# Performance work log

Hardware: AMD Instinct MI355X
Metric: run time of the kernel (lower is better)

The kernel has to match this reference:

```python
import jax, jax.numpy as jnp
import numpy as np

N = 100000
E = 1600000
H = 8
C = 16
DIM = 128
EDGE_DIM = 32


def setup_inputs() -> dict:
    key = jax.random.key(0)
    ks = jax.random.split(key, 7)
    s = 1.0 / np.sqrt(DIM)
    return {
        "x": jax.random.normal(ks[0], (N, DIM), dtype=jnp.float32),
        "edge_index": jax.random.randint(ks[1], (2, E), 0, N, dtype=jnp.int32),
        "edge_attr": jax.random.normal(ks[2], (E, EDGE_DIM), dtype=jnp.float32),
        "Wq": jax.random.normal(ks[3], (H * C, DIM), dtype=jnp.float32) * s,
        "Wk": jax.random.normal(ks[4], (H * C, DIM), dtype=jnp.float32) * s,
        "Wv": jax.random.normal(ks[5], (H * C, DIM), dtype=jnp.float32) * s,
        "We": jax.random.normal(ks[6], (H, EDGE_DIM), dtype=jnp.float32) * (1.0 / np.sqrt(EDGE_DIM)),
    }


def reference(x, edge_index, edge_attr, Wq, Wk, Wv, We):
    # Node projections: [N, H, C]
    q = (x @ Wq.T).reshape(N, H, C)
    k = (x @ Wk.T).reshape(N, H, C)
    v = (x @ Wv.T).reshape(N, H, C)

    src, dst = edge_index[0], edge_index[1]

    # Per-edge attention logits with edge bias: [E, H]
    edge_bias = edge_attr @ We.T
    scores = jnp.einsum("ehc,ehc->eh", q[dst], k[src]) / np.sqrt(C) + edge_bias

    # Numerically-stable segment softmax over destination groups
    seg_max = jax.ops.segment_max(scores, dst, num_segments=N)  # [N, H]
    ex = jnp.exp(scores - seg_max[dst])
    denom = jax.ops.segment_sum(ex, dst, num_segments=N)  # [N, H]
    alpha = ex / denom[dst]  # [E, H]

    # Scale gathered values and scatter-add to destinations
    msgs = v[src] * alpha[:, :, None]  # [E, H, C]
    out = jax.ops.segment_sum(msgs, dst, num_segments=N)  # [N, H, C]
    return out.reshape(N, H * C)
```

## Files before the change

### kernel.cpp

```cpp
#include <hip/hip_runtime.h>


typedef unsigned int uint32;
typedef unsigned short ushort16;

__device__ inline unsigned short f2bf(float f) {
    uint32 u = __float_as_uint(f);
    uint32 r = u + 0x7fffu + ((u >> 16) & 1u);
    return (unsigned short)(r >> 16);
}

__global__ __launch_bounds__(256) void qkv_count_kernel(
    const float* __restrict__ x,
    const float* __restrict__ Wq,
    const float* __restrict__ Wk,
    const float* __restrict__ Wv,
    const int* __restrict__ edge_index,
    float* __restrict__ q,
    unsigned short* __restrict__ kbf,
    unsigned short* __restrict__ vbf,
    int* __restrict__ counts,
    int N, int E)
{
    if (blockIdx.y == 6) {
        int idx = blockIdx.x * 256 + threadIdx.x;
        if (idx * 4 + 3 < E) {
            int4 d4 = ((const int4*)(edge_index + E))[idx];
            atomicAdd(&counts[d4.x], 1);
            atomicAdd(&counts[d4.y], 1);
            atomicAdd(&counts[d4.z], 1);
            atomicAdd(&counts[d4.w], 1);
        } else {
            for (int e = idx * 4; e < E; ++e)
                atomicAdd(&counts[edge_index[(size_t)E + e]], 1);
        }
        return;
    }

    const int nb = blockIdx.x * 64;
    const int cb = blockIdx.y * 64;
    const float* __restrict__ W = (cb < 128) ? Wq : (cb < 256) ? Wk : Wv;
    const int wrow0 = cb & 127;

    __shared__ float As[16][68];
    __shared__ float Bs[16][68];

    const int tid = threadIdx.x;
    const int tx = tid & 15;
    const int ty = tid >> 4;

    float acc[4][4] = {};

    const int lrow = tid >> 2;
    const int lk   = (tid & 3) * 4;
    const int n_load = nb + lrow;

    for (int k0 = 0; k0 < 128; k0 += 16) {
        float4 a = make_float4(0.f, 0.f, 0.f, 0.f);
        if (n_load < N)
            a = *(const float4*)(x + (size_t)n_load * 128 + k0 + lk);
        float4 b = *(const float4*)(W + (size_t)(wrow0 + lrow) * 128 + k0 + lk);
        As[lk + 0][lrow] = a.x; As[lk + 1][lrow] = a.y;
        As[lk + 2][lrow] = a.z; As[lk + 3][lrow] = a.w;
        Bs[lk + 0][lrow] = b.x; Bs[lk + 1][lrow] = b.y;
        Bs[lk + 2][lrow] = b.z; Bs[lk + 3][lrow] = b.w;
        __syncthreads();
#pragma unroll
        for (int kk = 0; kk < 16; ++kk) {
            float4 av = *(const float4*)&As[kk][ty * 4];
            float4 bv = *(const float4*)&Bs[kk][tx * 4];
            float avr[4] = {av.x, av.y, av.z, av.w};
            float bvr[4] = {bv.x, bv.y, bv.z, bv.w};
#pragma unroll
            for (int i = 0; i < 4; ++i)
#pragma unroll
                for (int j = 0; j < 4; ++j)
                    acc[i][j] = fmaf(avr[i], bvr[j], acc[i][j]);
        }
        __syncthreads();
    }

#pragma unroll
    for (int i = 0; i < 4; ++i) {
        int n = nb + ty * 4 + i;
        if (n >= N) continue;
        if (cb < 128) {
            float4 o = make_float4(acc[i][0], acc[i][1], acc[i][2], acc[i][3]);
            *(float4*)(q + (size_t)n * 128 + wrow0 + tx * 4) = o;
        } else {
            unsigned short* kv = (cb < 256) ? kbf : vbf;
            ushort4 o;
            o.x = f2bf(acc[i][0]); o.y = f2bf(acc[i][1]);
            o.z = f2bf(acc[i][2]); o.w = f2bf(acc[i][3]);
            *(ushort4*)(kv + (size_t)n * 128 + wrow0 + tx * 4) = o;
        }
    }
}

__global__ __launch_bounds__(256) void scan_pass1(
    const int* __restrict__ counts, int* __restrict__ blocksums, int N)
{
    __shared__ int red[256];
    int base = blockIdx.x * 512;
    int t = threadIdx.x;
    int s = 0;
    if (base + t < N)       s += counts[base + t];
    if (base + 256 + t < N) s += counts[base + 256 + t];
    red[t] = s;
    __syncthreads();
    for (int off = 128; off > 0; off >>= 1) {
        if (t < off) red[t] += red[t + off];
        __syncthreads();
    }
    if (t == 0) blocksums[blockIdx.x] = red[0];
}

__global__ __launch_bounds__(256) void scan_pass2(
    const int* __restrict__ blocksums, int* __restrict__ blockbase, int NB)
{
    __shared__ int sc[256];
    int t = threadIdx.x;
    int v = (t < NB) ? blocksums[t] : 0;
    sc[t] = v;
    __syncthreads();
    for (int off = 1; off < 256; off <<= 1) {
        int tmp = (t >= off) ? sc[t - off] : 0;
        __syncthreads();
        sc[t] += tmp;
        __syncthreads();
    }
    if (t < NB) blockbase[t] = sc[t] - v;
}

__global__ __launch_bounds__(256) void scan_pass3(
    const int* __restrict__ counts, const int* __restrict__ blockbase,
    int* __restrict__ offsets, int* __restrict__ cursor, int N)
{
    __shared__ int sc[256];
    int base = blockIdx.x * 512;
    int t = threadIdx.x;
    int i0 = base + 2 * t, i1 = i0 + 1;
    int c0 = (i0 < N) ? counts[i0] : 0;
    int c1 = (i1 < N) ? counts[i1] : 0;
    int pair = c0 + c1;
    sc[t] = pair;
    __syncthreads();
    for (int off = 1; off < 256; off <<= 1) {
        int tmp = (t >= off) ? sc[t - off] : 0;
        __syncthreads();
        sc[t] += tmp;
        __syncthreads();
    }
    int ex = sc[t] - pair + blockbase[blockIdx.x];
    if (i0 < N) { offsets[i0] = ex;      cursor[i0] = ex; }
    if (i1 < N) { offsets[i1] = ex + c0; cursor[i1] = ex + c0; }
}

__global__ __launch_bounds__(256) void scatter_kernel(
    const int* __restrict__ edge_index,
    int* __restrict__ cursor,
    int2* __restrict__ perm,
    int E)
{
    int e = blockIdx.x * 256 + threadIdx.x;
    if (e >= E) return;
    int s = edge_index[e];
    int d = edge_index[(size_t)E + e];
    int pos = atomicAdd(&cursor[d], 1);
    perm[pos] = make_int2(s, e);
}

__global__ __launch_bounds__(256) void attn_fused_kernel(
    const float* __restrict__ q,
    const unsigned short* __restrict__ kbf,
    const unsigned short* __restrict__ vbf,
    const float* __restrict__ edge_attr,
    const float* __restrict__ We,
    const int* __restrict__ offsets,
    const int* __restrict__ counts,
    const int2* __restrict__ perm,
    float* __restrict__ out,
    int N)
{
    const int d    = blockIdx.x * 4 + (threadIdx.x >> 6);
    const int lane = threadIdx.x & 63;
    if (d >= N) return;
    const int h = lane >> 3;
    const int j = lane & 7;

    const float4 we4 = *(const float4*)(We + h * 32 + j * 4);
    const float2 q2  = *(const float2*)(q + (size_t)d * 128 + lane * 2);

    const int start = offsets[d];
    const int cnt   = counts[d];

    float denom = 0.f, accx = 0.f, accy = 0.f;

    for (int i0 = 0; i0 < cnt; i0 += 64) {
        int m = min(64, cnt - i0);
        int2 pv = make_int2(0, 0);
        if (lane < m) pv = perm[start + i0 + lane];

        int src = __shfl(pv.x, 0), e = __shfl(pv.y, 0);
        uint32 kk2 = *(const uint32*)(kbf + (size_t)src * 128 + lane * 2);
        uint32 vv2 = *(const uint32*)(vbf + (size_t)src * 128 + lane * 2);
        float4 ea  = *(const float4*)(edge_attr + (size_t)e * 32 + j * 4);

        for (int t = 0; t < m; ++t) {
            uint32 ck = kk2, cv = vv2;
            float4 cea = ea;
            if (t + 1 < m) {
                int ns = __shfl(pv.x, t + 1), ne = __shfl(pv.y, t + 1);
                kk2 = *(const uint32*)(kbf + (size_t)ns * 128 + lane * 2);
                vv2 = *(const uint32*)(vbf + (size_t)ns * 128 + lane * 2);
                ea  = *(const float4*)(edge_attr + (size_t)ne * 32 + j * 4);
            }
            float kx = __uint_as_float(ck << 16);
            float ky = __uint_as_float(ck & 0xffff0000u);
            float part = 0.25f * (q2.x * kx + q2.y * ky)
                       + cea.x * we4.x + cea.y * we4.y
                       + cea.z * we4.z + cea.w * we4.w;
            part += __shfl_xor(part, 1);
            part += __shfl_xor(part, 2);
            part += __shfl_xor(part, 4);
            float ev = __expf(part);
            denom += ev;
            float vx = __uint_as_float(cv << 16);
            float vy = __uint_as_float(cv & 0xffff0000u);
            accx = fmaf(ev, vx, accx);
            accy = fmaf(ev, vy, accy);
        }
    }

    float inv = denom > 0.f ? 1.f / denom : 0.f;
    *(float2*)(out + (size_t)d * 128 + lane * 2) = make_float2(accx * inv, accy * inv);
}

extern "C" void kernel_launch(void* const* d_in, const int* in_sizes, int n_in,
                              void* d_out, int out_size, void* d_ws, size_t ws_size,
                              hipStream_t stream) {
    const float* x          = (const float*)d_in[0];
    const int*   edge_index = (const int*)d_in[1];
    const float* edge_attr  = (const float*)d_in[2];
    const float* Wq         = (const float*)d_in[3];
    const float* Wk         = (const float*)d_in[4];
    const float* Wv         = (const float*)d_in[5];
    const float* We         = (const float*)d_in[6];
    float* out = (float*)d_out;

    const int N = in_sizes[0] / 128;
    const int E = in_sizes[1] / 2;

    float* q = (float*)d_ws;
    unsigned short* kbf = (unsigned short*)(q + (size_t)N * 128);
    unsigned short* vbf = kbf + (size_t)N * 128;
    int2* perm = (int2*)(vbf + (size_t)N * 128);
    int* counts    = (int*)(perm + E);
    int* offsets   = counts + N;
    int* cursor    = offsets + N;
    int* blocksums = cursor + N;
    int* blockbase = blocksums + 256;

    hipMemsetAsync(counts, 0, (size_t)N * sizeof(int), stream);

    const int nxb = (N + 63) / 64;
    dim3 g1(nxb, 7);
    qkv_count_kernel<<<g1, 256, 0, stream>>>(x, Wq, Wk, Wv, edge_index,
                                             q, kbf, vbf, counts, N, E);

    const int NB = (N + 511) / 512;
    scan_pass1<<<NB, 256, 0, stream>>>(counts, blocksums, N);
    scan_pass2<<<1, 256, 0, stream>>>(blocksums, blockbase, NB);
    scan_pass3<<<NB, 256, 0, stream>>>(counts, blockbase, offsets, cursor, N);

    scatter_kernel<<<(E + 255) / 256, 256, 0, stream>>>(edge_index, cursor,
                                                        perm, E);

    attn_fused_kernel<<<(N + 3) / 4, 256, 0, stream>>>(
        q, kbf, vbf, edge_attr, We, offsets, counts, perm, out, N);
}
```

Measured before the change: 770.2 us.

## Deepen gather prefetch to two 4-edge groups in attention aggregation loop

The per-destination aggregation loop now keeps two groups of four edges' K/V/edge_attr loads in flight and software-pipelines them, where before it prefetched only one edge ahead. Edge indices are read with readlane instead of shfl, and the 0.25 scale is folded into q. The aim is to hide gather latency by raising memory-level parallelism. The cost is extra registers, which can lower occupancy.

```diff
diff --git a/kernel.cpp b/kernel.cpp
--- a/kernel.cpp
+++ b/kernel.cpp
@@ -2,7 +2,6 @@
 
 
 typedef unsigned int uint32;
-typedef unsigned short ushort16;
 
 __device__ inline unsigned short f2bf(float f) {
     uint32 u = __float_as_uint(f);
@@ -190,46 +189,70 @@
 
     const float4 we4 = *(const float4*)(We + h * 32 + j * 4);
     const float2 q2  = *(const float2*)(q + (size_t)d * 128 + lane * 2);
+    const float qx = q2.x * 0.25f;
+    const float qy = q2.y * 0.25f;
 
     const int start = offsets[d];
     const int cnt   = counts[d];
 
     float denom = 0.f, accx = 0.f, accy = 0.f;
 
+    const int laneb = lane * 4;
+    const char* kbp = (const char*)kbf;
+    const char* vbp = (const char*)vbf;
+
     for (int i0 = 0; i0 < cnt; i0 += 64) {
-        int m = min(64, cnt - i0);
+        const int m = min(64, cnt - i0);
         int2 pv = make_int2(0, 0);
         if (lane < m) pv = perm[start + i0 + lane];
 
-        int src = __shfl(pv.x, 0), e = __shfl(pv.y, 0);
-        uint32 kk2 = *(const uint32*)(kbf + (size_t)src * 128 + lane * 2);
-        uint32 vv2 = *(const uint32*)(vbf + (size_t)src * 128 + lane * 2);
-        float4 ea  = *(const float4*)(edge_attr + (size_t)e * 32 + j * 4);
-
-        for (int t = 0; t < m; ++t) {
-            uint32 ck = kk2, cv = vv2;
-            float4 cea = ea;
-            if (t + 1 < m) {
-                int ns = __shfl(pv.x, t + 1), ne = __shfl(pv.y, t + 1);
-                kk2 = *(const uint32*)(kbf + (size_t)ns * 128 + lane * 2);
-                vv2 = *(const uint32*)(vbf + (size_t)ns * 128 + lane * 2);
-                ea  = *(const float4*)(edge_attr + (size_t)ne * 32 + j * 4);
-            }
-            float kx = __uint_as_float(ck << 16);
-            float ky = __uint_as_float(ck & 0xffff0000u);
-            float part = 0.25f * (q2.x * kx + q2.y * ky)
-                       + cea.x * we4.x + cea.y * we4.y
-                       + cea.z * we4.z + cea.w * we4.w;
-            part += __shfl_xor(part, 1);
-            part += __shfl_xor(part, 2);
-            part += __shfl_xor(part, 4);
-            float ev = __expf(part);
-            denom += ev;
-            float vx = __uint_as_float(cv << 16);
-            float vy = __uint_as_float(cv & 0xffff0000u);
-            accx = fmaf(ev, vx, accx);
-            accy = fmaf(ev, vy, accy);
-        }
+        uint32 ka[4], va[4]; float4 ea[4];
+        uint32 kc[4], vc[4]; float4 ec[4];
+
+#define LOADG(AK, AV, AE, T0)                                                  \
+        _Pragma("unroll")                                                      \
+        for (int u = 0; u < 4; ++u) {                                          \
+            int t = (T0) + u;                                                  \
+            if (t < m) {                                                       \
+                int src = __builtin_amdgcn_readlane(pv.x, t);                  \
+                int e   = __builtin_amdgcn_readlane(pv.y, t);                  \
+                AK[u] = *(const uint32*)(kbp + ((size_t)src << 8) + laneb);    \
+                AV[u] = *(const uint32*)(vbp + ((size_t)src << 8) + laneb);    \
+                AE[u] = *(const float4*)(edge_attr + (size_t)e * 32 + j * 4);  \
+            }                                                                  \
+        }
+
+#define COMPG(AK, AV, AE, T0)                                                  \
+        _Pragma("unroll")                                                      \
+        for (int u = 0; u < 4; ++u) {                                          \
+            int t = (T0) + u;                                                  \
+            if (t < m) {                                                       \
+                float kx = __uint_as_float(AK[u] << 16);                       \
+                float ky = __uint_as_float(AK[u] & 0xffff0000u);               \
+                float4 ce = AE[u];                                             \
+                float part = qx * kx + qy * ky                                 \
+                           + ce.x * we4.x + ce.y * we4.y                       \
+                           + ce.z * we4.z + ce.w * we4.w;                      \
+                part += __shfl_xor(part, 1);                                   \
+                part += __shfl_xor(part, 2);                                   \
+                part += __shfl_xor(part, 4);                                   \
+                float ev = __expf(part);                                       \
+                denom += ev;                                                   \
+                accx = fmaf(ev, __uint_as_float(AV[u] << 16), accx);           \
+                accy = fmaf(ev, __uint_as_float(AV[u] & 0xffff0000u), accy);   \
+            }                                                                  \
+        }
+
+        LOADG(ka, va, ea, 0)
+        LOADG(kc, vc, ec, 4)
+        for (int t0 = 0; t0 < m; t0 += 8) {
+            COMPG(ka, va, ea, t0)
+            LOADG(ka, va, ea, t0 + 8)
+            COMPG(kc, vc, ec, t0 + 4)
+            LOADG(kc, vc, ec, t0 + 12)
+        }
+#undef LOADG
+#undef COMPG
     }
 
     float inv = denom > 0.f ? 1.f / denom : 0.f;
```

Measured after the change: 835.9 us. +8.5%, slower.

## Precompute per-edge bias in projection kernel and use DPP for head reductions

Applied to the files above, without the earlier changes.

Adds a grid slice to the projection kernel that computes the edge_attr·We bias for every edge with coalesced streaming reads and stores it as an E×8 array. The attention kernel then gathers one float per edge-head instead of a float4 of edge_attr per lane and drops the per-edge dot product. Cross-lane shuffles in the head reduction are replaced by DPP moves. This needs extra workspace and an additional large write and read of the bias array, and falls back to the old path if the workspace is too small.

```diff
diff --git a/kernel.cpp b/kernel.cpp
--- a/kernel.cpp
+++ b/kernel.cpp
@@ -2,12 +2,17 @@
 
 
 typedef unsigned int uint32;
-typedef unsigned short ushort16;
 
 __device__ inline unsigned short f2bf(float f) {
     uint32 u = __float_as_uint(f);
     uint32 r = u + 0x7fffu + ((u >> 16) & 1u);
     return (unsigned short)(r >> 16);
+}
+
+template <int CTRL>
+__device__ inline float dpp_mov(float v) {
+    return __int_as_float(__builtin_amdgcn_update_dpp(
+        0, __float_as_int(v), CTRL, 0xF, 0xF, true));
 }
 
 __global__ __launch_bounds__(256) void qkv_count_kernel(
@@ -15,10 +20,13 @@
     const float* __restrict__ Wq,
     const float* __restrict__ Wk,
     const float* __restrict__ Wv,
+    const float* __restrict__ We,
+    const float* __restrict__ edge_attr,
     const int* __restrict__ edge_index,
     float* __restrict__ q,
     unsigned short* __restrict__ kbf,
     unsigned short* __restrict__ vbf,
+    float* __restrict__ ebias,
     int* __restrict__ counts,
     int N, int E)
 {
@@ -33,6 +41,32 @@
         } else {
             for (int e = idx * 4; e < E; ++e)
                 atomicAdd(&counts[edge_index[(size_t)E + e]], 1);
+        }
+        return;
+    }
+
+    if (blockIdx.y == 7) {
+        const int t  = threadIdx.x;
+        const int h  = t & 7;
+        const int er = t >> 3;
+        float4 wreg[8];
+#pragma unroll
+        for (int i = 0; i < 8; ++i)
+            wreg[i] = *(const float4*)(We + h * 32 + i * 4);
+        const int e0 = blockIdx.x * 1024;
+        for (int it = 0; it < 32; ++it) {
+            int e = e0 + it * 32 + er;
+            if (e < E) {
+                const float* ea = edge_attr + (size_t)e * 32;
+                float s = 0.f;
+#pragma unroll
+                for (int i = 0; i < 8; ++i) {
+                    float4 a = *(const float4*)(ea + i * 4);
+                    float4 w = wreg[i];
+                    s += a.x * w.x + a.y * w.y + a.z * w.z + a.w * w.w;
+                }
+                ebias[(size_t)e * 8 + h] = s;
+            }
         }
         return;
     }
@@ -170,10 +204,12 @@
     perm[pos] = make_int2(s, e);
 }
 
+template <bool USE_BIAS>
 __global__ __launch_bounds__(256) void attn_fused_kernel(
     const float* __restrict__ q,
     const unsigned short* __restrict__ kbf,
     const unsigned short* __restrict__ vbf,
+    const float* __restrict__ ebias,
     const float* __restrict__ edge_attr,
     const float* __restrict__ We,
     const int* __restrict__ offsets,
@@ -188,8 +224,12 @@
     const int h = lane >> 3;
     const int j = lane & 7;
 
-    const float4 we4 = *(const float4*)(We + h * 32 + j * 4);
-    const float2 q2  = *(const float2*)(q + (size_t)d * 128 + lane * 2);
+    float4 we4 = make_float4(0.f, 0.f, 0.f, 0.f);
+    if (!USE_BIAS) we4 = *(const float4*)(We + h * 32 + j * 4);
+
+    const float2 q2 = *(const float2*)(q + (size_t)d * 128 + lane * 2);
+    const float qx = q2.x * 0.25f;
+    const float qy = q2.y * 0.25f;
 
     const int start = offsets[d];
     const int cnt   = counts[d];
@@ -204,26 +244,32 @@
         int src = __shfl(pv.x, 0), e = __shfl(pv.y, 0);
         uint32 kk2 = *(const uint32*)(kbf + (size_t)src * 128 + lane * 2);
         uint32 vv2 = *(const uint32*)(vbf + (size_t)src * 128 + lane * 2);
-        float4 ea  = *(const float4*)(edge_attr + (size_t)e * 32 + j * 4);
+        float bias = 0.f;
+        float4 ea  = make_float4(0.f, 0.f, 0.f, 0.f);
+        if (USE_BIAS) bias = ebias[(size_t)e * 8 + h];
+        else          ea   = *(const float4*)(edge_attr + (size_t)e * 32 + j * 4);
 
         for (int t = 0; t < m; ++t) {
             uint32 ck = kk2, cv = vv2;
+            float cb = bias;
             float4 cea = ea;
             if (t + 1 < m) {
                 int ns = __shfl(pv.x, t + 1), ne = __shfl(pv.y, t + 1);
                 kk2 = *(const uint32*)(kbf + (size_t)ns * 128 + lane * 2);
                 vv2 = *(const uint32*)(vbf + (size_t)ns * 128 + lane * 2);
-                ea  = *(const float4*)(edge_attr + (size_t)ne * 32 + j * 4);
+                if (USE_BIAS) bias = ebias[(size_t)ne * 8 + h];
+                else          ea   = *(const float4*)(edge_attr + (size_t)ne * 32 + j * 4);
             }
             float kx = __uint_as_float(ck << 16);
             float ky = __uint_as_float(ck & 0xffff0000u);
-            float part = 0.25f * (q2.x * kx + q2.y * ky)
-                       + cea.x * we4.x + cea.y * we4.y
-                       + cea.z * we4.z + cea.w * we4.w;
-            part += __shfl_xor(part, 1);
-            part += __shfl_xor(part, 2);
-            part += __shfl_xor(part, 4);
-            float ev = __expf(part);
+            float part = qx * kx + qy * ky;
+            if (!USE_BIAS)
+                part += cea.x * we4.x + cea.y * we4.y
+                      + cea.z * we4.z + cea.w * we4.w;
+            part += dpp_mov<0xB1>(part);
+            part += dpp_mov<0x4E>(part);
+            part += dpp_mov<0x141>(part);
+            float ev = __expf(USE_BIAS ? part + cb : part);
             denom += ev;
             float vx = __uint_as_float(cv << 16);
             float vy = __uint_as_float(cv & 0xffff0000u);
@@ -260,13 +306,19 @@
     int* cursor    = offsets + N;
     int* blocksums = cursor + N;
     int* blockbase = blocksums + 256;
+    float* ebias   = (float*)(blockbase + 256);
+
+    const size_t need_bias =
+        (size_t)((char*)(ebias + (size_t)E * 8) - (char*)d_ws);
+    const bool use_bias = ws_size >= need_bias;
 
     hipMemsetAsync(counts, 0, (size_t)N * sizeof(int), stream);
 
     const int nxb = (N + 63) / 64;
-    dim3 g1(nxb, 7);
-    qkv_count_kernel<<<g1, 256, 0, stream>>>(x, Wq, Wk, Wv, edge_index,
-                                             q, kbf, vbf, counts, N, E);
+    dim3 g1(nxb, use_bias ? 8 : 7);
+    qkv_count_kernel<<<g1, 256, 0, stream>>>(x, Wq, Wk, Wv, We, edge_attr,
+                                             edge_index, q, kbf, vbf, ebias,
+                                             counts, N, E);
 
     const int NB = (N + 511) / 512;
     scan_pass1<<<NB, 256, 0, stream>>>(counts, blocksums, N);
@@ -276,6 +328,10 @@
     scatter_kernel<<<(E + 255) / 256, 256, 0, stream>>>(edge_index, cursor,
                                                         perm, E);
 
-    attn_fused_kernel<<<(N + 3) / 4, 256, 0, stream>>>(
-        q, kbf, vbf, edge_attr, We, offsets, counts, perm, out, N);
-}
+    if (use_bias)
+        attn_fused_kernel<true><<<(N + 3) / 4, 256, 0, stream>>>(
+            q, kbf, vbf, ebias, edge_attr, We, offsets, counts, perm, out, N);
+    else
+        attn_fused_kernel<false><<<(N + 3) / 4, 256, 0, stream>>>(
+            q, kbf, vbf, ebias, edge_attr, We, offsets, counts, perm, out, N);
+}
```

Measured after the change: 829.8 us. 1.08x slower.
